# Optimization experiments

Measured on AMD Instinct MI355X. Metric: run time of the kernel, lower is better.

## Reference

```python
import jax, jax.numpy as jnp
import numpy as np

NEG_BIG = -9e15
ALPHA = 0.2  # LeakyReLU negative slope


def setup_inputs() -> dict:
    key = jax.random.key(0)
    k1, k2, k3, k4 = jax.random.split(key, 4)
    N, F_in, F_out = 8192, 256, 64
    inp = jax.random.normal(k1, (N, F_in), dtype=jnp.float32)
    adj = jax.random.randint(k2, (N, N), 0, 2, dtype=jnp.int32)
    W = jax.random.normal(k3, (F_in, F_out), dtype=jnp.float32) * 0.05
    a = jax.random.normal(k4, (2 * F_out, 1), dtype=jnp.float32) * 0.05
    return {"input": inp, "adj": adj, "W": W, "a": a}


def reference(input, adj, W, a):
    # h = X W : [N, F_out]
    h = input @ W
    F_out = W.shape[1]
    # a_input[i,j] = concat(h_i, h_j); a_input @ a = h@a1 broadcast over j + h@a2 broadcast over i.
    a1 = a[:F_out, 0]   # [F_out]
    a2 = a[F_out:, 0]   # [F_out]
    s1 = h @ a1         # [N]
    s2 = h @ a2         # [N]
    e = jax.nn.leaky_relu(s1[:, None] + s2[None, :], negative_slope=ALPHA)  # [N, N]
    att = jnp.where(adj > 0, e, jnp.float32(NEG_BIG))
    att = jax.nn.softmax(att, axis=1)
    # dropout is identity in eval mode (training=False)
    h_prime = att @ h   # [N, F_out]
    return jax.nn.elu(h_prime)
```

## Files before the change

kernel.cpp:

```cpp
#include <hip/hip_runtime.h>
#include <hip/hip_bf16.h>

typedef __bf16 bf16_t;
typedef __attribute__((ext_vector_type(8))) __bf16 bf16x8;
typedef __attribute__((ext_vector_type(4))) __bf16 bf16x4;
typedef __attribute__((ext_vector_type(4))) float floatx4;
typedef __attribute__((ext_vector_type(4))) int intx4;

#define NN 8192
#define FIN 256
#define FOUT 64
#define GAT_ALPHA 0.2f
#define JHALF (NN / 2)

__global__ __launch_bounds__(256) void gat_h_kernel(
    const float* __restrict__ input,
    const float* __restrict__ W,
    const float* __restrict__ a,
    bf16_t* __restrict__ hT,
    float* __restrict__ s1g, float* __restrict__ e1g, float* __restrict__ f1g,
    float* __restrict__ s2g, float* __restrict__ e2g, float* __restrict__ f2g)
{
    alignas(16) __shared__ bf16_t in_lds[32][264];
    alignas(16) __shared__ bf16_t wt_lds[64][264];
    __shared__ float h_lds[32][65];

    const int t  = threadIdx.x;
    const int i0 = blockIdx.x * 32;

    #pragma unroll
    for (int v = 0; v < 8; v++) {
        int u  = v * 256 + t;
        int i  = u >> 6;
        int k4 = (u & 63) * 4;
        floatx4 x = *(const floatx4*)(input + (size_t)(i0 + i) * FIN + k4);
        bf16x4 b;
        #pragma unroll
        for (int e = 0; e < 4; e++) b[e] = (bf16_t)x[e];
        *(bf16x4*)(&in_lds[i][k4]) = b;
    }
    #pragma unroll
    for (int v = 0; v < 16; v++) {
        int u  = v * 256 + t;
        int k  = u >> 4;
        int f4 = (u & 15) * 4;
        floatx4 wv = *(const floatx4*)(W + k * FOUT + f4);
        #pragma unroll
        for (int e = 0; e < 4; e++) wt_lds[f4 + e][k] = (bf16_t)wv[e];
    }
    __syncthreads();

    const int wave = t >> 6;
    const int lane = t & 63;
    const int i16  = (wave & 1) * 16;
    const int f32  = (wave >> 1) * 32;
    const int lm   = lane & 15;
    const int lq   = lane >> 4;

    floatx4 acc0 = {0.f, 0.f, 0.f, 0.f};
    floatx4 acc1 = {0.f, 0.f, 0.f, 0.f};
    #pragma unroll
    for (int ks = 0; ks < 8; ks++) {
        int ko = ks * 32 + lq * 8;
        bf16x8 af = *(const bf16x8*)(&in_lds[i16 + lm][ko]);
        bf16x8 b0 = *(const bf16x8*)(&wt_lds[f32 + lm][ko]);
        bf16x8 b1 = *(const bf16x8*)(&wt_lds[f32 + 16 + lm][ko]);
        acc0 = __builtin_amdgcn_mfma_f32_16x16x32_bf16(af, b0, acc0, 0, 0, 0);
        acc1 = __builtin_amdgcn_mfma_f32_16x16x32_bf16(af, b1, acc1, 0, 0, 0);
    }

    #pragma unroll
    for (int c = 0; c < 2; c++) {
        floatx4 acc = c ? acc1 : acc0;
        int f  = f32 + c * 16 + lm;
        int ib = i0 + i16 + lq * 4;
        bf16x4 hp;
        #pragma unroll
        for (int r = 0; r < 4; r++) hp[r] = (bf16_t)acc[r];
        *(bf16x4*)(hT + (size_t)f * NN + ib) = hp;
    }
    #pragma unroll
    for (int c = 0; c < 2; c++) {
        floatx4 acc = c ? acc1 : acc0;
        #pragma unroll
        for (int r = 0; r < 4; r++)
            h_lds[i16 + lq * 4 + r][f32 + c * 16 + lm] = acc[r];
    }
    __syncthreads();

    if (t < 64) {
        int r   = t & 31;
        int sel = t >> 5;
        const float* av = a + sel * FOUT;
        float s = 0.f;
        #pragma unroll 8
        for (int f = 0; f < FOUT; f++) s += h_lds[r][f] * av[f];
        int gi = i0 + r;
        float E = expf(s);
        float F = expf(GAT_ALPHA * s);
        if (sel == 0) { s1g[gi] = s; e1g[gi] = E; f1g[gi] = F; }
        else          { s2g[gi] = s; e2g[gi] = E; f2g[gi] = F; }
    }
}

#define LOAD_CHUNK(J0)                                                         \
    {                                                                          \
        s2v = *(const floatx4*)(s2g + (J0) + 4 * tj);                          \
        e2v = *(const floatx4*)(e2g + (J0) + 4 * tj);                          \
        f2v = *(const floatx4*)(f2g + (J0) + 4 * tj);                          \
        _Pragma("unroll")                                                      \
        for (int it = 0; it < 8; it++)                                         \
            adjv[it] = *(const intx4*)(adj +                                   \
                (size_t)(i0 + it * 4 + ti) * NN + (J0) + 4 * tj);              \
        _Pragma("unroll")                                                      \
        for (int u = 0; u < 8; u++) {                                          \
            int f  = (u * 256 + t) >> 5;                                       \
            int j8 = ((u * 256 + t) & 31) * 8;                                 \
            hv[u] = *(const bf16x8*)(hT + (size_t)f * NN + (J0) + j8);         \
        }                                                                      \
    }

#define CONSUME_CHUNK()                                                        \
    {                                                                          \
        _Pragma("unroll")                                                      \
        for (int it = 0; it < 8; it++) {                                       \
            int r = it * 4 + ti;                                               \
            float s1r = s1_l[r], E1 = e1_l[r], F1 = f1_l[r];                   \
            bf16x4 wq;                                                         \
            float sum = 0.f;                                                   \
            _Pragma("unroll")                                                  \
            for (int e = 0; e < 4; e++) {                                      \
                bool pos = (s1r + s2v[e]) > 0.f;                               \
                float wv = (adjv[it][e] > 0)                                   \
                               ? (pos ? E1 * e2v[e] : F1 * f2v[e]) : 0.f;      \
                bf16_t wb = (bf16_t)wv;                                        \
                wq[e] = wb;                                                    \
                sum += (float)wb;                                              \
            }                                                                  \
            rowsum[it] += sum;                                                 \
            *(bf16x4*)(&w_lds[r][4 * tj]) = wq;                                \
        }                                                                      \
        _Pragma("unroll")                                                      \
        for (int u = 0; u < 8; u++) {                                          \
            int f  = (u * 256 + t) >> 5;                                       \
            int j8 = ((u * 256 + t) & 31) * 8;                                 \
            *(bf16x8*)(&ht_lds[f][j8]) = hv[u];                                \
        }                                                                      \
    }

#define MFMA_CHUNK()                                                           \
    {                                                                          \
        _Pragma("unroll")                                                      \
        for (int ks = 0; ks < 8; ks++) {                                       \
            int ko = ks * 32 + lq * 8;                                         \
            bf16x8 af = *(const bf16x8*)(&w_lds[i16 + lm][ko]);                \
            bf16x8 b0 = *(const bf16x8*)(&ht_lds[f32 + lm][ko]);               \
            bf16x8 b1 = *(const bf16x8*)(&ht_lds[f32 + 16 + lm][ko]);          \
            acc0 = __builtin_amdgcn_mfma_f32_16x16x32_bf16(af, b0, acc0,0,0,0);\
            acc1 = __builtin_amdgcn_mfma_f32_16x16x32_bf16(af, b1, acc1,0,0,0);\
        }                                                                      \
    }

__global__ __launch_bounds__(256, 2) void gat_att_kernel(
    const int* __restrict__ adj,
    const bf16_t* __restrict__ hT,
    const float* __restrict__ s1g, const float* __restrict__ e1g,
    const float* __restrict__ f1g,
    const float* __restrict__ s2g, const float* __restrict__ e2g,
    const float* __restrict__ f2g,
    float* __restrict__ pacc,
    float* __restrict__ prs)
{
    alignas(16) __shared__ bf16_t w_lds[32][264];
    alignas(16) __shared__ bf16_t ht_lds[64][264];
    __shared__ float part[32][66];
    __shared__ float s1_l[32], e1_l[32], f1_l[32];

    const int t     = threadIdx.x;
    const int i0    = blockIdx.x * 32;
    const int half  = blockIdx.y;
    const int jbase = half * JHALF;
    const int tj    = t & 63;
    const int ti    = t >> 6;

    if (t < 32) {
        s1_l[t] = s1g[i0 + t];
        e1_l[t] = e1g[i0 + t];
        f1_l[t] = f1g[i0 + t];
    }

    const int wave = t >> 6;
    const int lane = t & 63;
    const int i16  = (wave & 1) * 16;
    const int f32  = (wave >> 1) * 32;
    const int lm   = lane & 15;
    const int lq   = lane >> 4;

    floatx4 acc0 = {0.f, 0.f, 0.f, 0.f};
    floatx4 acc1 = {0.f, 0.f, 0.f, 0.f};
    float rowsum[8];
    #pragma unroll
    for (int r = 0; r < 8; r++) rowsum[r] = 0.f;

    intx4   adjv[8];
    bf16x8  hv[8];
    floatx4 s2v, e2v, f2v;

    LOAD_CHUNK(jbase);

    for (int j0 = jbase; j0 < jbase + JHALF; j0 += 256) {
        __syncthreads();
        CONSUME_CHUNK();
        if (j0 + 256 < jbase + JHALF)
            LOAD_CHUNK(j0 + 256);
        __syncthreads();
        MFMA_CHUNK();
    }

    #pragma unroll
    for (int it = 0; it < 8; it++) part[it * 4 + ti][tj] = rowsum[it];
    __syncthreads();
    if (t < 32) {
        float s = 0.f;
        #pragma unroll 8
        for (int k = 0; k < 64; k++) s += part[t][k];
        prs[half * NN + i0 + t] = s;
    }

    float* pa = pacc + (size_t)half * NN * FOUT;
    #pragma unroll
    for (int c = 0; c < 2; c++) {
        floatx4 acc = c ? acc1 : acc0;
        int f = f32 + c * 16 + lm;
        #pragma unroll
        for (int r = 0; r < 4; r++) {
            int i = i16 + lq * 4 + r;
            pa[(size_t)(i0 + i) * FOUT + f] = acc[r];
        }
    }
}

__global__ __launch_bounds__(256) void gat_combine_kernel(
    const float* __restrict__ pacc,
    const float* __restrict__ prs,
    float* __restrict__ out)
{
    int idx = blockIdx.x * 256 + threadIdx.x;
    int i   = idx >> 4;
    floatx4 a0 = *(const floatx4*)(pacc + (size_t)idx * 4);
    floatx4 a1 = *(const floatx4*)(pacc + (size_t)NN * FOUT + (size_t)idx * 4);
    float rs   = prs[i] + prs[NN + i];
    float rinv = (rs > 0.f) ? 1.0f / rs : 0.f;
    floatx4 r;
    #pragma unroll
    for (int e = 0; e < 4; e++) {
        float x = (a0[e] + a1[e]) * rinv;
        r[e] = (x > 0.f) ? x : (expf(x) - 1.0f);
    }
    *(floatx4*)(out + (size_t)idx * 4) = r;
}

extern "C" void kernel_launch(void* const* d_in, const int* in_sizes, int n_in,
                              void* d_out, int out_size, void* d_ws, size_t ws_size,
                              hipStream_t stream) {
    const float* input = (const float*)d_in[0];
    const int*   adj   = (const int*)d_in[1];
    const float* W     = (const float*)d_in[2];
    const float* a     = (const float*)d_in[3];
    float*       out   = (float*)d_out;

    char* ws = (char*)d_ws;
    bf16_t* hT  = (bf16_t*)ws;
    float*  s1g = (float*)(ws + (1 << 20));
    float*  e1g = s1g + NN;
    float*  f1g = e1g + NN;
    float*  s2g = f1g + NN;
    float*  e2g = s2g + NN;
    float*  f2g = e2g + NN;
    float*  pacc = f2g + NN;
    float*  prs  = pacc + 2 * NN * FOUT;

    gat_h_kernel<<<NN / 32, 256, 0, stream>>>(input, W, a, hT,
                                              s1g, e1g, f1g, s2g, e2g, f2g);
    dim3 gridB(NN / 32, 2);
    gat_att_kernel<<<gridB, 256, 0, stream>>>(adj, hT,
                                              s1g, e1g, f1g, s2g, e2g, f2g,
                                              pacc, prs);
    gat_combine_kernel<<<NN * FOUT / 4 / 256, 256, 0, stream>>>(pacc, prs, out);
}
```

Baseline: 390.2 us.

## Build attention weights directly in MFMA registers and split columns into eight slices

The attention kernel now has each wave load adjacency and transposed-h fragments straight from global memory into registers, with X/Y double buffering. It computes the bf16 weights in the MFMA A-operand layout, which removes the LDS staging and the two barriers per chunk. The leaky-ReLU branch becomes a fmax of the two exponential products, and row sums come from an extra MFMA against a ones vector instead of a shared-memory reduction. The column range is split into eight slices, with 64-row blocks and more blocks per CU. The cost is more partial-sum traffic and a longer reduction in the combine kernel, plus hT fragments being reloaded from global memory by every row block.

```diff
diff --git a/kernel.cpp b/kernel.cpp
--- a/kernel.cpp
+++ b/kernel.cpp
@@ -11,7 +11,8 @@
 #define FIN 256
 #define FOUT 64
 #define GAT_ALPHA 0.2f
-#define JHALF (NN / 2)
+#define NSLICE 8
+#define JS (NN / NSLICE)
 
 __global__ __launch_bounds__(256) void gat_h_kernel(
     const float* __restrict__ input,
@@ -103,140 +104,109 @@
     }
 }
 
-#define LOAD_CHUNK(J0)                                                         \
-    {                                                                          \
-        s2v = *(const floatx4*)(s2g + (J0) + 4 * tj);                          \
-        e2v = *(const floatx4*)(e2g + (J0) + 4 * tj);                          \
-        f2v = *(const floatx4*)(f2g + (J0) + 4 * tj);                          \
-        _Pragma("unroll")                                                      \
-        for (int it = 0; it < 8; it++)                                         \
-            adjv[it] = *(const intx4*)(adj +                                   \
-                (size_t)(i0 + it * 4 + ti) * NN + (J0) + 4 * tj);              \
-        _Pragma("unroll")                                                      \
-        for (int u = 0; u < 8; u++) {                                          \
-            int f  = (u * 256 + t) >> 5;                                       \
-            int j8 = ((u * 256 + t) & 31) * 8;                                 \
-            hv[u] = *(const bf16x8*)(hT + (size_t)f * NN + (J0) + j8);         \
-        }                                                                      \
-    }
-
-#define CONSUME_CHUNK()                                                        \
-    {                                                                          \
-        _Pragma("unroll")                                                      \
-        for (int it = 0; it < 8; it++) {                                       \
-            int r = it * 4 + ti;                                               \
-            float s1r = s1_l[r], E1 = e1_l[r], F1 = f1_l[r];                   \
-            bf16x4 wq;                                                         \
-            float sum = 0.f;                                                   \
-            _Pragma("unroll")                                                  \
-            for (int e = 0; e < 4; e++) {                                      \
-                bool pos = (s1r + s2v[e]) > 0.f;                               \
-                float wv = (adjv[it][e] > 0)                                   \
-                               ? (pos ? E1 * e2v[e] : F1 * f2v[e]) : 0.f;      \
-                bf16_t wb = (bf16_t)wv;                                        \
-                wq[e] = wb;                                                    \
-                sum += (float)wb;                                              \
-            }                                                                  \
-            rowsum[it] += sum;                                                 \
-            *(bf16x4*)(&w_lds[r][4 * tj]) = wq;                                \
-        }                                                                      \
-        _Pragma("unroll")                                                      \
-        for (int u = 0; u < 8; u++) {                                          \
-            int f  = (u * 256 + t) >> 5;                                       \
-            int j8 = ((u * 256 + t) & 31) * 8;                                 \
-            *(bf16x8*)(&ht_lds[f][j8]) = hv[u];                                \
-        }                                                                      \
-    }
-
-#define MFMA_CHUNK()                                                           \
-    {                                                                          \
-        _Pragma("unroll")                                                      \
-        for (int ks = 0; ks < 8; ks++) {                                       \
-            int ko = ks * 32 + lq * 8;                                         \
-            bf16x8 af = *(const bf16x8*)(&w_lds[i16 + lm][ko]);                \
-            bf16x8 b0 = *(const bf16x8*)(&ht_lds[f32 + lm][ko]);               \
-            bf16x8 b1 = *(const bf16x8*)(&ht_lds[f32 + 16 + lm][ko]);          \
-            acc0 = __builtin_amdgcn_mfma_f32_16x16x32_bf16(af, b0, acc0,0,0,0);\
-            acc1 = __builtin_amdgcn_mfma_f32_16x16x32_bf16(af, b1, acc1,0,0,0);\
-        }                                                                      \
-    }
-
-__global__ __launch_bounds__(256, 2) void gat_att_kernel(
+#define LOADB(B, J)                                                           \
+    {                                                                         \
+        B##a0 = *(const intx4*)(adjp + (J));                                  \
+        B##a1 = *(const intx4*)(adjp + (J) + 4);                              \
+        B##h0 = *(const bf16x8*)(hp + (size_t)0  * NN + (J));                 \
+        B##h1 = *(const bf16x8*)(hp + (size_t)16 * NN + (J));                 \
+        B##h2 = *(const bf16x8*)(hp + (size_t)32 * NN + (J));                 \
+        B##h3 = *(const bf16x8*)(hp + (size_t)48 * NN + (J));                 \
+    }
+
+#define COMP(B, JL)                                                           \
+    {                                                                         \
+        int oo = (JL) + lq * 8;                                               \
+        floatx4 e2a = *(const floatx4*)(&e2l[oo]);                            \
+        floatx4 e2b = *(const floatx4*)(&e2l[oo + 4]);                        \
+        floatx4 f2a = *(const floatx4*)(&f2l[oo]);                            \
+        floatx4 f2b = *(const floatx4*)(&f2l[oo + 4]);                        \
+        bf16x8 frag;                                                          \
+        _Pragma("unroll")                                                     \
+        for (int e = 0; e < 4; e++) {                                         \
+            float w0 = fmaxf(E1 * e2a[e], F1 * f2a[e]);                       \
+            w0 = (B##a0[e] > 0) ? w0 : 0.f;                                   \
+            frag[e] = (bf16_t)w0;                                             \
+            float w1 = fmaxf(E1 * e2b[e], F1 * f2b[e]);                       \
+            w1 = (B##a1[e] > 0) ? w1 : 0.f;                                   \
+            frag[e + 4] = (bf16_t)w1;                                         \
+        }                                                                     \
+        acc0 = __builtin_amdgcn_mfma_f32_16x16x32_bf16(frag, B##h0, acc0,0,0,0); \
+        acc1 = __builtin_amdgcn_mfma_f32_16x16x32_bf16(frag, B##h1, acc1,0,0,0); \
+        acc2 = __builtin_amdgcn_mfma_f32_16x16x32_bf16(frag, B##h2, acc2,0,0,0); \
+        acc3 = __builtin_amdgcn_mfma_f32_16x16x32_bf16(frag, B##h3, acc3,0,0,0); \
+        accR = __builtin_amdgcn_mfma_f32_16x16x32_bf16(frag, ones, accR,0,0,0);  \
+    }
+
+__global__ __launch_bounds__(256, 4) void gat_att_kernel(
     const int* __restrict__ adj,
     const bf16_t* __restrict__ hT,
-    const float* __restrict__ s1g, const float* __restrict__ e1g,
-    const float* __restrict__ f1g,
-    const float* __restrict__ s2g, const float* __restrict__ e2g,
-    const float* __restrict__ f2g,
+    const float* __restrict__ e1g, const float* __restrict__ f1g,
+    const float* __restrict__ e2g, const float* __restrict__ f2g,
     float* __restrict__ pacc,
     float* __restrict__ prs)
 {
-    alignas(16) __shared__ bf16_t w_lds[32][264];
-    alignas(16) __shared__ bf16_t ht_lds[64][264];
-    __shared__ float part[32][66];
-    __shared__ float s1_l[32], e1_l[32], f1_l[32];
+    __shared__ float e2l[JS];
+    __shared__ float f2l[JS];
 
     const int t     = threadIdx.x;
-    const int i0    = blockIdx.x * 32;
-    const int half  = blockIdx.y;
-    const int jbase = half * JHALF;
-    const int tj    = t & 63;
-    const int ti    = t >> 6;
-
-    if (t < 32) {
-        s1_l[t] = s1g[i0 + t];
-        e1_l[t] = e1g[i0 + t];
-        f1_l[t] = f1g[i0 + t];
-    }
+    const int i0    = blockIdx.x * 64;
+    const int slice = blockIdx.y;
+    const int jbase = slice * JS;
+
+    {
+        int o = t * 4;
+        *(floatx4*)(&e2l[o]) = *(const floatx4*)(e2g + jbase + o);
+        *(floatx4*)(&f2l[o]) = *(const floatx4*)(f2g + jbase + o);
+    }
+    __syncthreads();
 
     const int wave = t >> 6;
     const int lane = t & 63;
-    const int i16  = (wave & 1) * 16;
-    const int f32  = (wave >> 1) * 32;
     const int lm   = lane & 15;
     const int lq   = lane >> 4;
-
-    floatx4 acc0 = {0.f, 0.f, 0.f, 0.f};
-    floatx4 acc1 = {0.f, 0.f, 0.f, 0.f};
-    float rowsum[8];
-    #pragma unroll
-    for (int r = 0; r < 8; r++) rowsum[r] = 0.f;
-
-    intx4   adjv[8];
-    bf16x8  hv[8];
-    floatx4 s2v, e2v, f2v;
-
-    LOAD_CHUNK(jbase);
-
-    for (int j0 = jbase; j0 < jbase + JHALF; j0 += 256) {
-        __syncthreads();
-        CONSUME_CHUNK();
-        if (j0 + 256 < jbase + JHALF)
-            LOAD_CHUNK(j0 + 256);
-        __syncthreads();
-        MFMA_CHUNK();
-    }
-
-    #pragma unroll
-    for (int it = 0; it < 8; it++) part[it * 4 + ti][tj] = rowsum[it];
-    __syncthreads();
-    if (t < 32) {
-        float s = 0.f;
-        #pragma unroll 8
-        for (int k = 0; k < 64; k++) s += part[t][k];
-        prs[half * NN + i0 + t] = s;
-    }
-
-    float* pa = pacc + (size_t)half * NN * FOUT;
-    #pragma unroll
-    for (int c = 0; c < 2; c++) {
-        floatx4 acc = c ? acc1 : acc0;
-        int f = f32 + c * 16 + lm;
-        #pragma unroll
-        for (int r = 0; r < 4; r++) {
-            int i = i16 + lq * 4 + r;
-            pa[(size_t)(i0 + i) * FOUT + f] = acc[r];
-        }
+    const int row  = i0 + wave * 16 + lm;
+
+    const float E1 = e1g[row];
+    const float F1 = f1g[row];
+
+    const int*    adjp = adj + (size_t)row * NN + jbase + lq * 8;
+    const bf16_t* hp   = hT + (size_t)lm * NN + jbase + lq * 8;
+
+    floatx4 acc0 = {0.f,0.f,0.f,0.f}, acc1 = {0.f,0.f,0.f,0.f};
+    floatx4 acc2 = {0.f,0.f,0.f,0.f}, acc3 = {0.f,0.f,0.f,0.f};
+    floatx4 accR = {0.f,0.f,0.f,0.f};
+
+    bf16x8 ones;
+    #pragma unroll
+    for (int e = 0; e < 8; e++) ones[e] = (bf16_t)1.0f;
+
+    intx4 Xa0, Xa1; bf16x8 Xh0, Xh1, Xh2, Xh3;
+    intx4 Ya0, Ya1; bf16x8 Yh0, Yh1, Yh2, Yh3;
+
+    LOADB(X, 0);
+    for (int jl = 0; jl < JS; jl += 64) {
+        int jn1 = jl + 32;
+        LOADB(Y, jn1);
+        COMP(X, jl);
+        int jn2 = (jl + 64 < JS) ? (jl + 64) : 0;
+        LOADB(X, jn2);
+        COMP(Y, jn1);
+    }
+
+    if (lm == 0) {
+        #pragma unroll
+        for (int r = 0; r < 4; r++)
+            prs[(size_t)slice * NN + i0 + wave * 16 + lq * 4 + r] = accR[r];
+    }
+
+    float* pa = pacc + (size_t)slice * NN * FOUT + (size_t)(i0 + wave * 16) * FOUT;
+    #pragma unroll
+    for (int c = 0; c < 4; c++) {
+        floatx4 acc = (c == 0) ? acc0 : (c == 1) ? acc1 : (c == 2) ? acc2 : acc3;
+        #pragma unroll
+        for (int r = 0; r < 4; r++)
+            pa[(size_t)(lq * 4 + r) * FOUT + c * 16 + lm] = acc[r];
     }
 }
 
@@ -247,14 +217,19 @@
 {
     int idx = blockIdx.x * 256 + threadIdx.x;
     int i   = idx >> 4;
-    floatx4 a0 = *(const floatx4*)(pacc + (size_t)idx * 4);
-    floatx4 a1 = *(const floatx4*)(pacc + (size_t)NN * FOUT + (size_t)idx * 4);
-    float rs   = prs[i] + prs[NN + i];
+    floatx4 s = {0.f, 0.f, 0.f, 0.f};
+    float rs  = 0.f;
+    #pragma unroll
+    for (int p = 0; p < NSLICE; p++) {
+        floatx4 v = *(const floatx4*)(pacc + (size_t)p * NN * FOUT + (size_t)idx * 4);
+        s += v;
+        rs += prs[p * NN + i];
+    }
     float rinv = (rs > 0.f) ? 1.0f / rs : 0.f;
     floatx4 r;
     #pragma unroll
     for (int e = 0; e < 4; e++) {
-        float x = (a0[e] + a1[e]) * rinv;
+        float x = s[e] * rinv;
         r[e] = (x > 0.f) ? x : (expf(x) - 1.0f);
     }
     *(floatx4*)(out + (size_t)idx * 4) = r;
@@ -278,13 +253,12 @@
     float*  e2g = s2g + NN;
     float*  f2g = e2g + NN;
     float*  pacc = f2g + NN;
-    float*  prs  = pacc + 2 * NN * FOUT;
+    float*  prs  = pacc + (size_t)NSLICE * NN * FOUT;
 
     gat_h_kernel<<<NN / 32, 256, 0, stream>>>(input, W, a, hT,
                                               s1g, e1g, f1g, s2g, e2g, f2g);
-    dim3 gridB(NN / 32, 2);
-    gat_att_kernel<<<gridB, 256, 0, stream>>>(adj, hT,
-                                              s1g, e1g, f1g, s2g, e2g, f2g,
+    dim3 gridB(NN / 64, NSLICE);
+    gat_att_kernel<<<gridB, 256, 0, stream>>>(adj, hT, e1g, f1g, e2g, f2g,
                                               pacc, prs);
     gat_combine_kernel<<<NN * FOUT / 4 / 256, 256, 0, stream>>>(pacc, prs, out);
 }
```

New measurement: 438.8 us. 1.12x slower.
